# Kernel tuning notes

Hardware: AMD Instinct MI355X
Metric: run time of the kernel (lower is better)

The kernel has to match this reference:

```python
import jax, jax.numpy as jnp
import numpy as np


def setup_inputs() -> dict:
    key = jax.random.key(0)
    ks = jax.random.split(key, 10)
    T, D, E, K, H = 16384, 1024, 8, 2, 4096
    scale = 0.02
    return {
        "x_flat": jax.random.normal(ks[0], (T, D), jnp.float32),
        "noise": jax.random.normal(ks[1], (T, E), jnp.float32),
        "gate_w": jax.random.normal(ks[2], (E, D), jnp.float32) * scale,
        "noise_weight": jnp.zeros((E,), jnp.float32),
        "w1": jax.random.normal(ks[3], (E, H, D), jnp.float32) * scale,
        "b1": jnp.zeros((E, H), jnp.float32),
        "w2": jax.random.normal(ks[4], (E, H, D), jnp.float32) * scale,
        "b2": jnp.zeros((E, H), jnp.float32),
        "wp": jax.random.normal(ks[5], (E, D, H), jnp.float32) * scale,
        "bp": jnp.zeros((E, D), jnp.float32),
    }


K_TOP = 2
LOAD_BALANCE_SCALE = 0.01


def reference(x_flat, noise, gate_w, noise_weight, w1, b1, w2, b2, wp, bp):
    T, D = x_flat.shape
    E = gate_w.shape[0]
    # ---- gate ----
    logits = x_flat @ gate_w.T                        # [T, E]
    gate_weights = jax.nn.softmax(logits, axis=-1)    # [T, E]
    gw_mean = gate_weights.mean(axis=0)               # [E]
    uniform = jnp.ones_like(gw_mean) / E
    load_balance_loss = jnp.mean((gw_mean - uniform) ** 2) * LOAD_BALANCE_SCALE
    # noisy top-k (noise_weight initialized to zeros => noise is a no-op, kept for faithfulness)
    logits_noisy = logits + noise * noise_weight
    top_v, top_i = jax.lax.top_k(logits_noisy, K_TOP)  # [T, K]
    neg_inf = jnp.full_like(logits_noisy, -jnp.inf)
    sparse = neg_inf.at[jnp.arange(T)[:, None], top_i].set(top_v)
    top_k_gated_weights = jax.nn.softmax(sparse, axis=-1)  # [T, E], zero off top-k
    # ---- experts (SwiGLU), weighted combine ----
    # Non-top-k weights are exactly 0, so a dense masked sum over experts equals
    # the original gather/grouped-GEMM/scatter dispatch on a single device.
    y = jnp.zeros_like(x_flat)
    for e in range(E):
        h = x_flat @ w1[e].T + b1[e]                  # [T, H]
        g = jax.nn.silu(x_flat @ w2[e].T + b2[e])     # [T, H]
        out_e = (h * g) @ wp[e].T + bp[e]             # [T, D]
        y = y + top_k_gated_weights[:, e:e + 1] * out_e
    return y, load_balance_loss
```

## Files before the change

### kernel.cpp

```cpp
#include <hip/hip_runtime.h>
#include <hip/hip_bf16.h>

#define T_TOK 16384
#define DDIM  1024
#define NEXP  8
#define HDIM  4096
#define HQ    1024
#define NQ    4
#define TOTR  (2 * T_TOK)

#define BM 128
#define BK 64

typedef __attribute__((ext_vector_type(8))) short bf16x8;
typedef __attribute__((ext_vector_type(4))) float f32x4;

__device__ __forceinline__ unsigned short f2bf(float f) {
  unsigned int x = __builtin_bit_cast(unsigned int, f);
  x += 0x7fffu + ((x >> 16) & 1u);
  return (unsigned short)(x >> 16);
}
__device__ __forceinline__ void gload16(void* lds, const void* g) {
  __builtin_amdgcn_global_load_lds(
      (const __attribute__((address_space(1))) unsigned int*)g,
      (__attribute__((address_space(3))) unsigned int*)lds, 16, 0, 0);
}
__device__ __forceinline__ f32x4 mfma16(bf16x8 a, bf16x8 b, f32x4 c) {
  return __builtin_amdgcn_mfma_f32_16x16x32_bf16(a, b, c, 0, 0, 0);
}

#define OFF_GWSUM  ((size_t)0)
#define OFF_OFF16  ((size_t)64)
#define OFF_NP     ((size_t)128)
#define OFF_BLK    ((size_t)1024)
#define OFF_GBASE  ((size_t)8192)
#define OFF_PEXPP  ((size_t)16384)
#define OFF_PM0P   ((size_t)18432)
#define OFF_PENDP  ((size_t)20480)
#define OFF_PEXPS  ((size_t)22528)
#define OFF_PM0S   ((size_t)24576)
#define OFF_PENDS  ((size_t)26624)
#define OFF_TOPE   ((size_t)32768)
#define OFF_TOPW   (OFF_TOPE   + (size_t)T_TOK*2*4)
#define OFF_LRANK  (OFF_TOPW   + (size_t)T_TOK*2*4)
#define OFF_ROWTOK (OFF_LRANK  + (size_t)T_TOK*4)
#define OFF_ROWG   (OFF_ROWTOK + (size_t)T_TOK*2*4)
#define OFF_XG     ((size_t)1 << 20)
#define OFF_ACTQ   (OFF_XG   + (size_t)TOTR*DDIM*2)
#define OFF_W1Q    (OFF_ACTQ + (size_t)TOTR*HQ*2)
#define OFF_W2Q    (OFF_W1Q  + (size_t)NEXP*HQ*DDIM*2)
#define OFF_WPQ    (OFF_W2Q  + (size_t)NEXP*HQ*DDIM*2)
#define WS_NEEDED  (OFF_WPQ  + (size_t)NEXP*DDIM*HQ*2 + ((size_t)1<<20))

__global__ __launch_bounds__(256) void k_gate(
    const float* __restrict__ x, const float* __restrict__ noise,
    const float* __restrict__ gate_w, const float* __restrict__ nw,
    float* __restrict__ gwsum, int* __restrict__ tope, float* __restrict__ topw)
{
  __shared__ float gw_s[NEXP * DDIM];
  __shared__ float blk_gw[NEXP];
  const int tid = threadIdx.x;
  if (tid < NEXP) blk_gw[tid] = 0.f;
  {
    float4* dst = (float4*)gw_s;
    const float4* src = (const float4*)gate_w;
    for (int i = tid; i < NEXP * DDIM / 4; i += 256) dst[i] = src[i];
  }
  __syncthreads();

  const int wv = tid >> 6, lane = tid & 63;
  const int t = blockIdx.x * 4 + wv;

  const float4* xr = (const float4*)(x + (size_t)t * DDIM);
  float4 xv[4];
  #pragma unroll
  for (int c = 0; c < 4; ++c) xv[c] = xr[lane + 64 * c];

  float logit[NEXP];
  #pragma unroll
  for (int e = 0; e < NEXP; ++e) {
    float p = 0.f;
    const float4* g4 = (const float4*)(gw_s + e * DDIM);
    #pragma unroll
    for (int c = 0; c < 4; ++c) {
      float4 g = g4[lane + 64 * c];
      p += xv[c].x * g.x + xv[c].y * g.y + xv[c].z * g.z + xv[c].w * g.w;
    }
    #pragma unroll
    for (int off = 32; off >= 1; off >>= 1) p += __shfl_xor(p, off, 64);
    logit[e] = p;
  }

  if (lane == 0) {
    float m = logit[0];
    #pragma unroll
    for (int e = 1; e < NEXP; ++e) m = fmaxf(m, logit[e]);
    float sm[NEXP]; float s = 0.f;
    #pragma unroll
    for (int e = 0; e < NEXP; ++e) { sm[e] = expf(logit[e] - m); s += sm[e]; }
    float inv = 1.f / s;
    #pragma unroll
    for (int e = 0; e < NEXP; ++e) atomicAdd(&blk_gw[e], sm[e] * inv);

    float ln[NEXP];
    #pragma unroll
    for (int e = 0; e < NEXP; ++e) ln[e] = logit[e] + noise[(size_t)t * NEXP + e] * nw[e];
    int i1 = 0; float v1 = ln[0];
    #pragma unroll
    for (int e = 1; e < NEXP; ++e) if (ln[e] > v1) { v1 = ln[e]; i1 = e; }
    int i2 = -1; float v2 = -3.4e38f;
    #pragma unroll
    for (int e = 0; e < NEXP; ++e) if (e != i1 && ln[e] > v2) { v2 = ln[e]; i2 = e; }
    float b = expf(v2 - v1);
    float wsum = 1.f + b;
    tope[2 * t] = i1; tope[2 * t + 1] = i2;
    topw[2 * t] = 1.f / wsum; topw[2 * t + 1] = b / wsum;
  }
  __syncthreads();
  if (tid < NEXP) atomicAdd(&gwsum[tid], blk_gw[tid]);
}

__global__ __launch_bounds__(256) void k_hist(
    const int* __restrict__ tope, unsigned int* __restrict__ lrank,
    int* __restrict__ blkcnt)
{
  __shared__ int cnt16[16];
  const int tid = threadIdx.x;
  const int t = blockIdx.x * 256 + tid;
  if (tid < 16) cnt16[tid] = 0;
  __syncthreads();
  const int e0 = tope[2 * t], e1 = tope[2 * t + 1];
  const int b0 = 2 * e0 + (e0 < e1 ? 0 : 1);
  const int b1 = 2 * e1 + (e1 < e0 ? 0 : 1);
  const int lr0 = atomicAdd(&cnt16[b0], 1);
  const int lr1 = atomicAdd(&cnt16[b1], 1);
  lrank[t] = (unsigned int)lr0 | ((unsigned int)lr1 << 16);
  __syncthreads();
  if (tid < 16) blkcnt[blockIdx.x * 16 + tid] = cnt16[tid];
}

__global__ __launch_bounds__(512) void k_scan(
    const int* __restrict__ blkcnt, int* __restrict__ gbase,
    int* __restrict__ off16, int* __restrict__ np,
    int* __restrict__ pexpP, int* __restrict__ pm0P, int* __restrict__ pendP,
    int* __restrict__ pexpS, int* __restrict__ pm0S, int* __restrict__ pendS,
    const float* __restrict__ gwsum, float* __restrict__ out_loss)
{
  __shared__ int ld[64][16];
  __shared__ int sc[64][16];
  __shared__ int tot[16];
  __shared__ int o16[16];
  const int tid = threadIdx.x;
  for (int i = tid; i < 1024; i += 512) ld[i >> 4][i & 15] = blkcnt[i];
  __syncthreads();
  if (tid < 16) {
    int run = 0;
    for (int i = 0; i < 64; ++i) { sc[i][tid] = run; run += ld[i][tid]; }
    tot[tid] = run;
  }
  __syncthreads();
  if (tid == 0) {
    int o = 0;
    for (int b = 0; b < 16; ++b) { o16[b] = o; off16[b] = o; o += tot[b]; }
    int nP = 0, nS = 0;
    for (int b = 0; b < 16; ++b) {
      const int e = b >> 1, s = b & 1;
      const int beg = o16[b], end = beg + tot[b];
      for (int m = beg; m < end; m += BM) {
        const int me = (m + BM < end) ? (m + BM) : end;
        if (!s) { pexpP[nP] = e; pm0P[nP] = m; pendP[nP] = me; ++nP; }
        else    { pexpS[nS] = e; pm0S[nS] = m; pendS[nS] = me; ++nS; }
      }
    }
    np[0] = nP; np[1] = nS;
    float s = 0.f;
    for (int i = 0; i < NEXP; ++i) {
      float d = gwsum[i] / (float)T_TOK - 1.f / (float)NEXP;
      s += d * d;
    }
    out_loss[0] = (s / (float)NEXP) * 0.01f;
  }
  __syncthreads();
  for (int i = tid; i < 1024; i += 512)
    gbase[i] = o16[i & 15] + sc[i >> 4][i & 15];
}

__global__ __launch_bounds__(256) void k_copy(
    const float* __restrict__ x, const int* __restrict__ tope,
    const float* __restrict__ topw, const unsigned int* __restrict__ lrank,
    const int* __restrict__ gbase,
    int* __restrict__ rowtok, float* __restrict__ rowgate,
    unsigned short* __restrict__ Xg)
{
  const int tid = threadIdx.x;
  const int wv = tid >> 6, lane = tid & 63;
  const int t = blockIdx.x * 4 + wv;
  const int e0 = tope[2 * t], e1 = tope[2 * t + 1];
  const int b0 = 2 * e0 + (e0 < e1 ? 0 : 1);
  const int b1 = 2 * e1 + (e1 < e0 ? 0 : 1);
  const unsigned int lr = lrank[t];
  const int hb = t >> 8;
  const int r0 = gbase[hb * 16 + b0] + (int)(lr & 0xffffu);
  const int r1 = gbase[hb * 16 + b1] + (int)(lr >> 16);
  if (lane == 0) {
    rowtok[r0] = t; rowtok[r1] = t;
    rowgate[r0] = topw[2 * t]; rowgate[r1] = topw[2 * t + 1];
  }
  const float4* xr = (const float4*)(x + (size_t)t * DDIM);
  ushort4 o[4];
  #pragma unroll
  for (int c = 0; c < 4; ++c) {
    float4 v = xr[lane + 64 * c];
    o[c].x = f2bf(v.x); o[c].y = f2bf(v.y); o[c].z = f2bf(v.z); o[c].w = f2bf(v.w);
  }
  ushort4* d0 = (ushort4*)(Xg + (size_t)r0 * DDIM);
  ushort4* d1 = (ushort4*)(Xg + (size_t)r1 * DDIM);
  #pragma unroll
  for (int c = 0; c < 4; ++c) d0[lane + 64 * c] = o[c];
  #pragma unroll
  for (int c = 0; c < 4; ++c) d1[lane + 64 * c] = o[c];
}

__global__ __launch_bounds__(256) void k_castall(
    const float* __restrict__ w1, const float* __restrict__ w2,
    const float* __restrict__ wp,
    unsigned short* __restrict__ w1q, unsigned short* __restrict__ w2q,
    unsigned short* __restrict__ wpq, int q)
{
  const int N4 = NEXP * HQ * DDIM / 4;
  for (int i = blockIdx.x * 256 + threadIdx.x; i < 3 * N4; i += gridDim.x * 256) {
    int j = i;
    float4 v; size_t dstIdx; unsigned short* d;
    if (j < N4) {
      const int c4 = j & 255, rr = j >> 8, e = rr >> 10, r = rr & 1023;
      v = ((const float4*)w1)[((size_t)e * HDIM + q * HQ + r) * 256 + c4];
      d = w1q; dstIdx = (size_t)rr * 256 + c4;
    } else if (j < 2 * N4) {
      j -= N4;
      const int c4 = j & 255, rr = j >> 8, e = rr >> 10, r = rr & 1023;
      v = ((const float4*)w2)[((size_t)e * HDIM + q * HQ + r) * 256 + c4];
      d = w2q; dstIdx = (size_t)rr * 256 + c4;
    } else {
      j -= 2 * N4;
      const int c4 = j & 255, rr = j >> 8;
      v = ((const float4*)wp)[(size_t)rr * 1024 + q * 256 + c4];
      d = wpq; dstIdx = (size_t)rr * 256 + c4;
    }
    ushort4 o;
    o.x = f2bf(v.x); o.y = f2bf(v.y); o.z = f2bf(v.z); o.w = f2bf(v.w);
    ((ushort4*)d)[dstIdx] = o;
  }
}

#define FBN 64
#define FGX 280
#define FGY 16
__global__ __launch_bounds__(256, 2) void k_fused(
    const unsigned short* __restrict__ Xg,
    const unsigned short* __restrict__ w1q, const unsigned short* __restrict__ w2q,
    const float* __restrict__ b1, const float* __restrict__ b2,
    unsigned short* __restrict__ actq, const int* __restrict__ np,
    const int* __restrict__ pexpP, const int* __restrict__ pm0P, const int* __restrict__ pendP,
    const int* __restrict__ pexpS, const int* __restrict__ pm0S, const int* __restrict__ pendS,
    int q)
{
  const int flat = blockIdx.y * FGX + blockIdx.x;
  const int CPX = (FGX * FGY) / 8;
  const int L = (flat & 7) * CPX + (flat >> 3);
  const int pidx = L >> 4;
  const int yc = L & 15;
  const int nP = np[0], nS = np[1];
  int e, m0, mend;
  if (pidx < nP)            { e = pexpP[pidx]; m0 = pm0P[pidx]; mend = pendP[pidx]; }
  else if (pidx < nP + nS)  { int s = pidx - nP; e = pexpS[s]; m0 = pm0S[s]; mend = pendS[s]; }
  else return;

  __shared__ unsigned short As[BM * BK];
  __shared__ unsigned short B1s[FBN * BK];
  __shared__ unsigned short B2s[FBN * BK];

  const int tid = threadIdx.x;
  const int wid = tid >> 6, lane = tid & 63;
  const int wr = wid >> 1, wc = wid & 1;
  const int fr = lane & 15;
  const int fq = lane >> 4;

  const unsigned short* Bbase1 = w1q + ((size_t)e * HQ + yc * FBN) * DDIM;
  const unsigned short* Bbase2 = w2q + ((size_t)e * HQ + yc * FBN) * DDIM;

  f32x4 acc1[4][2] = {};
  f32x4 acc2[4][2] = {};

  for (int kt = 0; kt < DDIM / BK; ++kt) {
    if (kt > 0) __syncthreads();
    const int k0 = kt * BK;
    #pragma unroll
    for (int it = 0; it < 4; ++it) {
      const int idx = it * 256 + tid;
      const int row = idx >> 3, seg = idx & 7;
      const int koff = ((seg ^ (row & 7)) << 3);
      int arow = m0 + row; if (arow >= TOTR) arow = TOTR - 1;
      gload16(&As[idx * 8], Xg + (size_t)arow * DDIM + k0 + koff);
    }
    #pragma unroll
    for (int it = 0; it < 2; ++it) {
      const int idx = it * 256 + tid;
      const int row = idx >> 3, seg = idx & 7;
      const int koff = ((seg ^ (row & 7)) << 3);
      gload16(&B1s[idx * 8], Bbase1 + (size_t)row * DDIM + k0 + koff);
    }
    #pragma unroll
    for (int it = 0; it < 2; ++it) {
      const int idx = it * 256 + tid;
      const int row = idx >> 3, seg = idx & 7;
      const int koff = ((seg ^ (row & 7)) << 3);
      gload16(&B2s[idx * 8], Bbase2 + (size_t)row * DDIM + k0 + koff);
    }
    __syncthreads();

    #pragma unroll
    for (int kk = 0; kk < 2; ++kk) {
      bf16x8 b1v[2], b2v[2];
      #pragma unroll
      for (int nf = 0; nf < 2; ++nf) {
        const int row = wc * 32 + nf * 16 + fr;
        const int seg = (kk * 4 + fq) ^ (row & 7);
        b1v[nf] = *(const bf16x8*)&B1s[row * BK + seg * 8];
        b2v[nf] = *(const bf16x8*)&B2s[row * BK + seg * 8];
      }
      #pragma unroll
      for (int mf = 0; mf < 4; ++mf) {
        const int row = wr * 64 + mf * 16 + fr;
        const int seg = (kk * 4 + fq) ^ (row & 7);
        bf16x8 av = *(const bf16x8*)&As[row * BK + seg * 8];
        #pragma unroll
        for (int nf = 0; nf < 2; ++nf) {
          acc1[mf][nf] = mfma16(av, b1v[nf], acc1[mf][nf]);
          acc2[mf][nf] = mfma16(av, b2v[nf], acc2[mf][nf]);
        }
      }
    }
  }

  const int mcnt = mend - m0;
  #pragma unroll
  for (int mf = 0; mf < 4; ++mf) {
    const int rb = wr * 64 + mf * 16 + (fq << 2);
    #pragma unroll
    for (int nf = 0; nf < 2; ++nf) {
      const int cq = yc * FBN + wc * 32 + nf * 16 + fr;
      const float bb1 = b1[(size_t)e * HDIM + q * HQ + cq];
      const float bb2 = b2[(size_t)e * HDIM + q * HQ + cq];
      #pragma unroll
      for (int j = 0; j < 4; ++j) {
        const int lr = rb + j;
        if (lr < mcnt) {
          float h = acc1[mf][nf][j] + bb1;
          float g = acc2[mf][nf][j] + bb2;
          float s = g / (1.f + expf(-g));
          actq[(size_t)(m0 + lr) * HQ + cq] = f2bf(h * s);
        }
      }
    }
  }
}

#define DBN 64
#define DGX 144
#define DGY 8
template<bool STORE>
__global__ __launch_bounds__(256, 2) void k_down(
    const unsigned short* __restrict__ actq, const unsigned short* __restrict__ wpq,
    const float* __restrict__ bp,
    const int* __restrict__ np, int npIdx,
    const int* __restrict__ pexp, const int* __restrict__ pm0, const int* __restrict__ pend,
    const int* __restrict__ rowtok, const float* __restrict__ rowgate,
    float* __restrict__ Y)
{
  const int flat = blockIdx.y * DGX + blockIdx.x;
  const int CPX = (DGX * DGY) / 8;
  const int L = (flat & 7) * CPX + (flat >> 3);
  const int pidx = L >> 3;
  const int yc = L & 7;
  if (pidx >= np[npIdx]) return;
  const int e = pexp[pidx], m0 = pm0[pidx], mend = pend[pidx];

  __shared__ unsigned short As[BM * BK];
  __shared__ unsigned short Bs1[DBN * BK];
  __shared__ unsigned short Bs2[DBN * BK];

  const int tid = threadIdx.x;
  const int wid = tid >> 6, lane = tid & 63;
  const int wr = wid >> 1, wc = wid & 1;
  const int fr = lane & 15;
  const int fq = lane >> 4;

  const unsigned short* Bbase1 = wpq + ((size_t)e * DDIM + yc * 128) * HQ;
  const unsigned short* Bbase2 = Bbase1 + (size_t)64 * HQ;

  f32x4 acc1[4][2] = {};
  f32x4 acc2[4][2] = {};

  for (int kt = 0; kt < HQ / BK; ++kt) {
    if (kt > 0) __syncthreads();
    const int k0 = kt * BK;
    #pragma unroll
    for (int it = 0; it < 4; ++it) {
      const int idx = it * 256 + tid;
      const int row = idx >> 3, seg = idx & 7;
      const int koff = ((seg ^ (row & 7)) << 3);
      int arow = m0 + row; if (arow >= TOTR) arow = TOTR - 1;
      gload16(&As[idx * 8], actq + (size_t)arow * HQ + k0 + koff);
    }
    #pragma unroll
    for (int it = 0; it < 2; ++it) {
      const int idx = it * 256 + tid;
      const int row = idx >> 3, seg = idx & 7;
      const int koff = ((seg ^ (row & 7)) << 3);
      gload16(&Bs1[idx * 8], Bbase1 + (size_t)row * HQ + k0 + koff);
    }
    #pragma unroll
    for (int it = 0; it < 2; ++it) {
      const int idx = it * 256 + tid;
      const int row = idx >> 3, seg = idx & 7;
      const int koff = ((seg ^ (row & 7)) << 3);
      gload16(&Bs2[idx * 8], Bbase2 + (size_t)row * HQ + k0 + koff);
    }
    __syncthreads();

    #pragma unroll
    for (int kk = 0; kk < 2; ++kk) {
      bf16x8 b1v[2], b2v[2];
      #pragma unroll
      for (int nf = 0; nf < 2; ++nf) {
        const int row = wc * 32 + nf * 16 + fr;
        const int seg = (kk * 4 + fq) ^ (row & 7);
        b1v[nf] = *(const bf16x8*)&Bs1[row * BK + seg * 8];
        b2v[nf] = *(const bf16x8*)&Bs2[row * BK + seg * 8];
      }
      #pragma unroll
      for (int mf = 0; mf < 4; ++mf) {
        const int row = wr * 64 + mf * 16 + fr;
        const int seg = (kk * 4 + fq) ^ (row & 7);
        bf16x8 av = *(const bf16x8*)&As[row * BK + seg * 8];
        #pragma unroll
        for (int nf = 0; nf < 2; ++nf) {
          acc1[mf][nf] = mfma16(av, b1v[nf], acc1[mf][nf]);
          acc2[mf][nf] = mfma16(av, b2v[nf], acc2[mf][nf]);
        }
      }
    }
  }

  const int mcnt = mend - m0;
  #pragma unroll
  for (int mf = 0; mf < 4; ++mf) {
    const int rb = wr * 64 + mf * 16 + (fq << 2);
    #pragma unroll
    for (int nf = 0; nf < 2; ++nf) {
      const int dg1 = yc * 128 + wc * 32 + nf * 16 + fr;
      const int dg2 = dg1 + 64;
      const float bb1 = bp[(size_t)e * DDIM + dg1];
      const float bb2 = bp[(size_t)e * DDIM + dg2];
      #pragma unroll
      for (int j = 0; j < 4; ++j) {
        const int lr = rb + j;
        if (lr < mcnt) {
          const int r = m0 + lr;
          const float gt = rowgate[r];
          float* yrow = &Y[(size_t)rowtok[r] * DDIM];
          const float o1 = gt * (acc1[mf][nf][j] + bb1);
          const float o2 = gt * (acc2[mf][nf][j] + bb2);
          if (STORE) { yrow[dg1] = o1; yrow[dg2] = o2; }
          else       { yrow[dg1] += o1; yrow[dg2] += o2; }
        }
      }
    }
  }
}

extern "C" void kernel_launch(void* const* d_in, const int* in_sizes, int n_in,
                              void* d_out, int out_size, void* d_ws, size_t ws_size,
                              hipStream_t stream) {
  const float* x      = (const float*)d_in[0];
  const float* noise  = (const float*)d_in[1];
  const float* gate_w = (const float*)d_in[2];
  const float* nw     = (const float*)d_in[3];
  const float* w1     = (const float*)d_in[4];
  const float* b1     = (const float*)d_in[5];
  const float* w2     = (const float*)d_in[6];
  const float* b2     = (const float*)d_in[7];
  const float* wp     = (const float*)d_in[8];
  const float* bp     = (const float*)d_in[9];
  float* y = (float*)d_out;

  if (ws_size < WS_NEEDED) return;

  char* ws = (char*)d_ws;
  float* gwsum   = (float*)(ws + OFF_GWSUM);
  int*   off16   = (int*)(ws + OFF_OFF16);
  int*   np      = (int*)(ws + OFF_NP);
  int*   blkcnt  = (int*)(ws + OFF_BLK);
  int*   gbase   = (int*)(ws + OFF_GBASE);
  int*   pexpP   = (int*)(ws + OFF_PEXPP);
  int*   pm0P    = (int*)(ws + OFF_PM0P);
  int*   pendP   = (int*)(ws + OFF_PENDP);
  int*   pexpS   = (int*)(ws + OFF_PEXPS);
  int*   pm0S    = (int*)(ws + OFF_PM0S);
  int*   pendS   = (int*)(ws + OFF_PENDS);
  int*   tope    = (int*)(ws + OFF_TOPE);
  float* topw    = (float*)(ws + OFF_TOPW);
  unsigned int* lrank = (unsigned int*)(ws + OFF_LRANK);
  int*   rowtok  = (int*)(ws + OFF_ROWTOK);
  float* rowgate = (float*)(ws + OFF_ROWG);
  unsigned short* Xg   = (unsigned short*)(ws + OFF_XG);
  unsigned short* actq = (unsigned short*)(ws + OFF_ACTQ);
  unsigned short* w1q  = (unsigned short*)(ws + OFF_W1Q);
  unsigned short* w2q  = (unsigned short*)(ws + OFF_W2Q);
  unsigned short* wpq  = (unsigned short*)(ws + OFF_WPQ);

  hipMemsetAsync(d_ws, 0, 64, stream);

  k_gate<<<T_TOK / 4, 256, 0, stream>>>(x, noise, gate_w, nw, gwsum, tope, topw);
  k_hist<<<T_TOK / 256, 256, 0, stream>>>(tope, lrank, blkcnt);
  k_scan<<<1, 512, 0, stream>>>(blkcnt, gbase, off16, np,
                                pexpP, pm0P, pendP, pexpS, pm0S, pendS,
                                gwsum, y + (size_t)T_TOK * DDIM);
  k_copy<<<T_TOK / 4, 256, 0, stream>>>(x, tope, topw, lrank, gbase,
                                        rowtok, rowgate, Xg);

  for (int q = 0; q < NQ; ++q) {
    k_castall<<<3072, 256, 0, stream>>>(w1, w2, wp, w1q, w2q, wpq, q);
    k_fused<<<dim3(FGX, FGY), 256, 0, stream>>>(
        Xg, w1q, w2q, b1, b2, actq, np,
        pexpP, pm0P, pendP, pexpS, pm0S, pendS, q);
    if (q == 0)
      k_down<true><<<dim3(DGX, DGY), 256, 0, stream>>>(
          actq, wpq, bp, np, 0, pexpP, pm0P, pendP, rowtok, rowgate, y);
    else
      k_down<false><<<dim3(DGX, DGY), 256, 0, stream>>>(
          actq, wpq, bp, np, 0, pexpP, pm0P, pendP, rowtok, rowgate, y);
    k_down<false><<<dim3(DGX, DGY), 256, 0, stream>>>(
        actq, wpq, bp, np, 1, pexpS, pm0S, pendS, rowtok, rowgate, y);
  }
}
```

Baseline: 1.663 ms.

## Rebuild fused up-projection kernel with 256x128 tiles and software-pipelined double-buffered LDS

```diff
diff --git a/kernel.cpp b/kernel.cpp
--- a/kernel.cpp
+++ b/kernel.cpp
@@ -29,11 +29,22 @@
   return __builtin_amdgcn_mfma_f32_16x16x32_bf16(a, b, c, 0, 0, 0);
 }
 
+#define BARR  __builtin_amdgcn_s_barrier()
+#define LGKM0 do { asm volatile("s_waitcnt lgkmcnt(0)" ::: "memory"); \
+                   __builtin_amdgcn_sched_barrier(0); } while (0)
+#define VMW(n) do { asm volatile("s_waitcnt vmcnt(" #n ")" ::: "memory"); \
+                    __builtin_amdgcn_sched_barrier(0); } while (0)
+#define PRIO1 __builtin_amdgcn_s_setprio(1)
+#define PRIO0 __builtin_amdgcn_s_setprio(0)
+
 #define OFF_GWSUM  ((size_t)0)
 #define OFF_OFF16  ((size_t)64)
 #define OFF_NP     ((size_t)128)
 #define OFF_BLK    ((size_t)1024)
 #define OFF_GBASE  ((size_t)8192)
+#define OFF_PEXPF  ((size_t)12288)
+#define OFF_PM0F   ((size_t)13312)
+#define OFF_PENDF  ((size_t)14336)
 #define OFF_PEXPP  ((size_t)16384)
 #define OFF_PM0P   ((size_t)18432)
 #define OFF_PENDP  ((size_t)20480)
@@ -144,6 +155,7 @@
     int* __restrict__ off16, int* __restrict__ np,
     int* __restrict__ pexpP, int* __restrict__ pm0P, int* __restrict__ pendP,
     int* __restrict__ pexpS, int* __restrict__ pm0S, int* __restrict__ pendS,
+    int* __restrict__ pexpF, int* __restrict__ pm0F, int* __restrict__ pendF,
     const float* __restrict__ gwsum, float* __restrict__ out_loss)
 {
   __shared__ int ld[64][16];
@@ -162,7 +174,7 @@
   if (tid == 0) {
     int o = 0;
     for (int b = 0; b < 16; ++b) { o16[b] = o; off16[b] = o; o += tot[b]; }
-    int nP = 0, nS = 0;
+    int nP = 0, nS = 0, nF = 0;
     for (int b = 0; b < 16; ++b) {
       const int e = b >> 1, s = b & 1;
       const int beg = o16[b], end = beg + tot[b];
@@ -171,8 +183,12 @@
         if (!s) { pexpP[nP] = e; pm0P[nP] = m; pendP[nP] = me; ++nP; }
         else    { pexpS[nS] = e; pm0S[nS] = m; pendS[nS] = me; ++nS; }
       }
-    }
-    np[0] = nP; np[1] = nS;
+      for (int m = beg; m < end; m += 256) {
+        pexpF[nF] = e; pm0F[nF] = m;
+        pendF[nF] = (m + 256 < end) ? (m + 256) : end; ++nF;
+      }
+    }
+    np[0] = nP; np[1] = nS; np[2] = nF;
     float s = 0.f;
     for (int i = 0; i < NEXP; ++i) {
       float d = gwsum[i] / (float)T_TOK - 1.f / (float)NEXP;
@@ -252,112 +268,140 @@
   }
 }
 
-#define FBN 64
-#define FGX 280
-#define FGY 16
-__global__ __launch_bounds__(256, 2) void k_fused(
+#define FGXN 144
+__global__ __launch_bounds__(512, 2) void k_fused(
     const unsigned short* __restrict__ Xg,
     const unsigned short* __restrict__ w1q, const unsigned short* __restrict__ w2q,
     const float* __restrict__ b1, const float* __restrict__ b2,
     unsigned short* __restrict__ actq, const int* __restrict__ np,
-    const int* __restrict__ pexpP, const int* __restrict__ pm0P, const int* __restrict__ pendP,
-    const int* __restrict__ pexpS, const int* __restrict__ pm0S, const int* __restrict__ pendS,
-    int q)
-{
-  const int flat = blockIdx.y * FGX + blockIdx.x;
-  const int CPX = (FGX * FGY) / 8;
+    const int* __restrict__ pexpF, const int* __restrict__ pm0F,
+    const int* __restrict__ pendF, int q)
+{
+  extern __shared__ unsigned short lds[];
+  const int flat = blockIdx.y * FGXN + blockIdx.x;
+  const int CPX = (FGXN * 8) / 8;
   const int L = (flat & 7) * CPX + (flat >> 3);
-  const int pidx = L >> 4;
-  const int yc = L & 15;
-  const int nP = np[0], nS = np[1];
-  int e, m0, mend;
-  if (pidx < nP)            { e = pexpP[pidx]; m0 = pm0P[pidx]; mend = pendP[pidx]; }
-  else if (pidx < nP + nS)  { int s = pidx - nP; e = pexpS[s]; m0 = pm0S[s]; mend = pendS[s]; }
-  else return;
-
-  __shared__ unsigned short As[BM * BK];
-  __shared__ unsigned short B1s[FBN * BK];
-  __shared__ unsigned short B2s[FBN * BK];
+  const int pidx = L >> 3;
+  const int yc = L & 7;
+  if (pidx >= np[2]) return;
+  const int e = pexpF[pidx], m0 = pm0F[pidx], mend = pendF[pidx];
 
   const int tid = threadIdx.x;
   const int wid = tid >> 6, lane = tid & 63;
-  const int wr = wid >> 1, wc = wid & 1;
-  const int fr = lane & 15;
-  const int fq = lane >> 4;
-
-  const unsigned short* Bbase1 = w1q + ((size_t)e * HQ + yc * FBN) * DDIM;
-  const unsigned short* Bbase2 = w2q + ((size_t)e * HQ + yc * FBN) * DDIM;
-
-  f32x4 acc1[4][2] = {};
-  f32x4 acc2[4][2] = {};
-
-  for (int kt = 0; kt < DDIM / BK; ++kt) {
-    if (kt > 0) __syncthreads();
-    const int k0 = kt * BK;
-    #pragma unroll
-    for (int it = 0; it < 4; ++it) {
-      const int idx = it * 256 + tid;
-      const int row = idx >> 3, seg = idx & 7;
-      const int koff = ((seg ^ (row & 7)) << 3);
+  const int wm = wid >> 2, wn = wid & 3;
+  const int wmb = wm * 128, wnb = wn * 32;
+  const int fr = lane & 15, fq = lane >> 4;
+  const int rsw = ((fq ^ (fr & 3)) << 3);
+
+  const unsigned short* Bw1 = w1q + ((size_t)e * HQ + yc * 128) * DDIM;
+  const unsigned short* Bw2 = w2q + ((size_t)e * HQ + yc * 128) * DDIM;
+
+  f32x4 acc1[8][2] = {};
+  f32x4 acc2[8][2] = {};
+  bf16x8 aA[8], wf[2];
+
+  auto stA = [&](int slot, int kk, int kt) {
+    #pragma unroll
+    for (int l = 0; l < 2; ++l) {
+      const int idx = l * 512 + tid;
+      const int row = idx >> 2, seg = idx & 3;
+      const int koff = kt * 64 + kk * 32 + ((seg ^ (row & 3)) << 3);
       int arow = m0 + row; if (arow >= TOTR) arow = TOTR - 1;
-      gload16(&As[idx * 8], Xg + (size_t)arow * DDIM + k0 + koff);
-    }
-    #pragma unroll
-    for (int it = 0; it < 2; ++it) {
-      const int idx = it * 256 + tid;
-      const int row = idx >> 3, seg = idx & 7;
-      const int koff = ((seg ^ (row & 7)) << 3);
-      gload16(&B1s[idx * 8], Bbase1 + (size_t)row * DDIM + k0 + koff);
-    }
-    #pragma unroll
-    for (int it = 0; it < 2; ++it) {
-      const int idx = it * 256 + tid;
-      const int row = idx >> 3, seg = idx & 7;
-      const int koff = ((seg ^ (row & 7)) << 3);
-      gload16(&B2s[idx * 8], Bbase2 + (size_t)row * DDIM + k0 + koff);
-    }
-    __syncthreads();
-
-    #pragma unroll
-    for (int kk = 0; kk < 2; ++kk) {
-      bf16x8 b1v[2], b2v[2];
+      gload16(&lds[slot * 32768 + kk * 8192 + idx * 8],
+              Xg + (size_t)arow * DDIM + koff);
+    }
+  };
+  auto stW = [&](int slot, int mat, int kk, int kt, const unsigned short* B) {
+    const int row = tid >> 2, seg = tid & 3;
+    const int koff = kt * 64 + kk * 32 + ((seg ^ (row & 3)) << 3);
+    gload16(&lds[slot * 32768 + 16384 + mat * 8192 + kk * 4096 + tid * 8],
+            B + (size_t)row * DDIM + koff);
+  };
+  auto rdA8 = [&](int slot, int kk) {
+    #pragma unroll
+    for (int mf = 0; mf < 8; ++mf) {
+      const int row = wmb + mf * 16 + fr;
+      aA[mf] = *(const bf16x8*)&lds[slot * 32768 + kk * 8192 + row * 32 + rsw];
+    }
+  };
+  auto rdW = [&](int slot, int mat, int kk) {
+    #pragma unroll
+    for (int nf = 0; nf < 2; ++nf) {
+      const int row = wnb + nf * 16 + fr;
+      wf[nf] = *(const bf16x8*)
+          &lds[slot * 32768 + 16384 + mat * 8192 + kk * 4096 + row * 32 + rsw];
+    }
+  };
+  auto MF1 = [&]() {
+    PRIO1;
+    #pragma unroll
+    for (int mf = 0; mf < 8; ++mf)
       #pragma unroll
-      for (int nf = 0; nf < 2; ++nf) {
-        const int row = wc * 32 + nf * 16 + fr;
-        const int seg = (kk * 4 + fq) ^ (row & 7);
-        b1v[nf] = *(const bf16x8*)&B1s[row * BK + seg * 8];
-        b2v[nf] = *(const bf16x8*)&B2s[row * BK + seg * 8];
-      }
+      for (int nf = 0; nf < 2; ++nf)
+        acc1[mf][nf] = mfma16(aA[mf], wf[nf], acc1[mf][nf]);
+    PRIO0;
+  };
+  auto MF2 = [&]() {
+    PRIO1;
+    #pragma unroll
+    for (int mf = 0; mf < 8; ++mf)
       #pragma unroll
-      for (int mf = 0; mf < 4; ++mf) {
-        const int row = wr * 64 + mf * 16 + fr;
-        const int seg = (kk * 4 + fq) ^ (row & 7);
-        bf16x8 av = *(const bf16x8*)&As[row * BK + seg * 8];
-        #pragma unroll
-        for (int nf = 0; nf < 2; ++nf) {
-          acc1[mf][nf] = mfma16(av, b1v[nf], acc1[mf][nf]);
-          acc2[mf][nf] = mfma16(av, b2v[nf], acc2[mf][nf]);
-        }
-      }
-    }
-  }
+      for (int nf = 0; nf < 2; ++nf)
+        acc2[mf][nf] = mfma16(aA[mf], wf[nf], acc2[mf][nf]);
+    PRIO0;
+  };
+
+  stA(0, 0, 0); stW(0, 0, 0, 0, Bw1); stW(0, 1, 0, 0, Bw2);
+  stA(0, 1, 0); stW(0, 0, 1, 0, Bw1); stW(0, 1, 1, 0, Bw2);
+  stA(1, 0, 1); stW(1, 0, 0, 1, Bw1); stW(1, 1, 0, 1, Bw2); stW(1, 0, 1, 1, Bw1);
+  VMW(10); BARR;
+
+  for (int i = 0; i < 7; ++i) {
+    const int t1 = 2 * i + 1, t2 = 2 * i + 2, t3 = 2 * i + 3;
+    rdA8(0, 0); rdW(0, 0, 0); stA(1, 1, t1); stW(1, 1, 1, t1, Bw2);
+    LGKM0; MF1(); VMW(10); BARR;
+    rdW(0, 1, 0); stW(0, 0, 0, t2, Bw1);
+    LGKM0; MF2(); VMW(10); BARR;
+    rdA8(0, 1); rdW(0, 0, 1); stA(0, 0, t2); stW(0, 1, 0, t2, Bw2);
+    LGKM0; MF1(); VMW(10); BARR;
+    rdW(0, 1, 1); stW(0, 0, 1, t2, Bw1);
+    LGKM0; MF2(); VMW(10); BARR;
+    rdA8(1, 0); rdW(1, 0, 0); stA(0, 1, t2); stW(0, 1, 1, t2, Bw2);
+    LGKM0; MF1(); VMW(10); BARR;
+    rdW(1, 1, 0); stW(1, 0, 0, t3, Bw1);
+    LGKM0; MF2(); VMW(10); BARR;
+    rdA8(1, 1); rdW(1, 0, 1); stA(1, 0, t3); stW(1, 1, 0, t3, Bw2);
+    LGKM0; MF1(); VMW(10); BARR;
+    rdW(1, 1, 1); stW(1, 0, 1, t3, Bw1);
+    LGKM0; MF2(); VMW(10); BARR;
+  }
+
+  rdA8(0, 0); rdW(0, 0, 0); stA(1, 1, 15); stW(1, 1, 1, 15, Bw2);
+  LGKM0; MF1(); VMW(0); BARR;
+  rdW(0, 1, 0); LGKM0; MF2();
+  rdA8(0, 1); rdW(0, 0, 1); LGKM0; MF1();
+  rdW(0, 1, 1); LGKM0; MF2();
+  rdA8(1, 0); rdW(1, 0, 0); LGKM0; MF1();
+  rdW(1, 1, 0); LGKM0; MF2();
+  rdA8(1, 1); rdW(1, 0, 1); LGKM0; MF1();
+  rdW(1, 1, 1); LGKM0; MF2();
 
   const int mcnt = mend - m0;
   #pragma unroll
-  for (int mf = 0; mf < 4; ++mf) {
-    const int rb = wr * 64 + mf * 16 + (fq << 2);
+  for (int mf = 0; mf < 8; ++mf) {
+    const int rb = wmb + mf * 16 + (fq << 2);
     #pragma unroll
     for (int nf = 0; nf < 2; ++nf) {
-      const int cq = yc * FBN + wc * 32 + nf * 16 + fr;
+      const int cq = yc * 128 + wnb + nf * 16 + fr;
       const float bb1 = b1[(size_t)e * HDIM + q * HQ + cq];
       const float bb2 = b2[(size_t)e * HDIM + q * HQ + cq];
       #pragma unroll
       for (int j = 0; j < 4; ++j) {
         const int lr = rb + j;
         if (lr < mcnt) {
-          float h = acc1[mf][nf][j] + bb1;
-          float g = acc2[mf][nf][j] + bb2;
-          float s = g / (1.f + expf(-g));
+          const float h = acc1[mf][nf][j] + bb1;
+          const float g = acc2[mf][nf][j] + bb2;
+          const float s = g / (1.f + expf(-g));
           actq[(size_t)(m0 + lr) * HQ + cq] = f2bf(h * s);
         }
       }
@@ -502,6 +546,9 @@
   int*   np      = (int*)(ws + OFF_NP);
   int*   blkcnt  = (int*)(ws + OFF_BLK);
   int*   gbase   = (int*)(ws + OFF_GBASE);
+  int*   pexpF   = (int*)(ws + OFF_PEXPF);
+  int*   pm0F    = (int*)(ws + OFF_PM0F);
+  int*   pendF   = (int*)(ws + OFF_PENDF);
   int*   pexpP   = (int*)(ws + OFF_PEXPP);
   int*   pm0P    = (int*)(ws + OFF_PM0P);
   int*   pendP   = (int*)(ws + OFF_PENDP);
@@ -525,15 +572,16 @@
   k_hist<<<T_TOK / 256, 256, 0, stream>>>(tope, lrank, blkcnt);
   k_scan<<<1, 512, 0, stream>>>(blkcnt, gbase, off16, np,
                                 pexpP, pm0P, pendP, pexpS, pm0S, pendS,
+                                pexpF, pm0F, pendF,
                                 gwsum, y + (size_t)T_TOK * DDIM);
   k_copy<<<T_TOK / 4, 256, 0, stream>>>(x, tope, topw, lrank, gbase,
                                         rowtok, rowgate, Xg);
 
+  const size_t LDSB = 131072;
   for (int q = 0; q < NQ; ++q) {
     k_castall<<<3072, 256, 0, stream>>>(w1, w2, wp, w1q, w2q, wpq, q);
-    k_fused<<<dim3(FGX, FGY), 256, 0, stream>>>(
-        Xg, w1q, w2q, b1, b2, actq, np,
-        pexpP, pm0P, pendP, pexpS, pm0S, pendS, q);
+    k_fused<<<dim3(FGXN, 8), 512, LDSB, stream>>>(
+        Xg, w1q, w2q, b1, b2, actq, np, pexpF, pm0F, pendF, q);
     if (q == 0)
       k_down<true><<<dim3(DGX, DGY), 256, 0, stream>>>(
           actq, wpq, bp, np, 0, pexpP, pm0P, pendP, rowtok, rowgate, y);
```

Result: slower. 1.723 ms (+3.6%).
